# Kernel optimization log

Hardware: AMD Instinct MI355X
Metric: run time of the kernel (lower is better)

The kernel has to match this reference:

```python
import jax, jax.numpy as jnp
import numpy as np

HIDDEN = 2048
HEADS = 16
HEAD_DIM = HIDDEN // HEADS
BLOCK = 64
SEQ = 4096
NUM_BLOCKS = SEQ // BLOCK
N_LOCAL = 3
N_GLOBAL = 1
N_RANDOM = 1
SCALE = 1.0 / np.sqrt(HEAD_DIM)


def _sparse_mask(rand_idx):
    # rand_idx: [num_blocks, n_random] int -- random key-block per query-block row
    i = jnp.arange(NUM_BLOCKS)[:, None]
    j = jnp.arange(NUM_BLOCKS)[None, :]
    half = N_LOCAL // 2
    local = (j >= i - half) & (j <= i + half)
    glob = (j < N_GLOBAL) | (j >= NUM_BLOCKS - N_GLOBAL)
    rand = jnp.any(j[:, :, None] == rand_idx[:, None, :], axis=-1)
    blk = local | glob | rand                      # [nb, nb] bool
    full = jnp.repeat(jnp.repeat(blk, BLOCK, axis=0), BLOCK, axis=1)
    return full[:SEQ, :SEQ]                        # [S, S] bool


def setup_inputs() -> dict:
    key = jax.random.key(0)
    k1, k2, k3, k4, k5, k6 = jax.random.split(key, 6)
    s = 0.02
    return {
        "hidden_states": jax.random.normal(k1, (1, SEQ, HIDDEN), jnp.float32),
        "rand_idx": jax.random.randint(k2, (NUM_BLOCKS, N_RANDOM), 0, NUM_BLOCKS, jnp.int32),
        "Wq": jax.random.normal(k3, (HIDDEN, HIDDEN), jnp.float32) * s,
        "Wk": jax.random.normal(k4, (HIDDEN, HIDDEN), jnp.float32) * s,
        "Wv": jax.random.normal(k5, (HIDDEN, HIDDEN), jnp.float32) * s,
        "Wo": jax.random.normal(k6, (HIDDEN, HIDDEN), jnp.float32) * s,
    }


def reference(hidden_states, rand_idx, Wq, Wk, Wv, Wo):
    B, S, _ = hidden_states.shape
    # torch Linear: y = x @ W.T
    q = (hidden_states @ Wq.T).reshape(B, S, HEADS, HEAD_DIM).transpose(0, 2, 1, 3)
    k = (hidden_states @ Wk.T).reshape(B, S, HEADS, HEAD_DIM).transpose(0, 2, 1, 3)
    v = (hidden_states @ Wv.T).reshape(B, S, HEADS, HEAD_DIM).transpose(0, 2, 1, 3)
    scores = jnp.einsum("bhqd,bhkd->bhqk", q, k) * SCALE
    mask = _sparse_mask(rand_idx)                  # [S, S] bool
    scores = jnp.where(mask[None, None, :, :], scores, -jnp.inf)
    probs = jax.nn.softmax(scores, axis=-1)
    out = jnp.einsum("bhqk,bhkd->bhqd", probs, v)
    out = out.transpose(0, 2, 1, 3).reshape(B, S, HIDDEN)
    return out @ Wo.T
```

## Files before the change

### kernel.cpp

```cpp
#include <hip/hip_runtime.h>

typedef unsigned short u16;
typedef __bf16 bf16x8 __attribute__((ext_vector_type(8)));
typedef float f32x4 __attribute__((ext_vector_type(4)));

#define SEQQ 4096
#define HID 2048
#define HD 128
#define NBLK 64
#define ATT_SCALE 0.08838834764831843f

__device__ __forceinline__ u16 f2bf(float f) {
    unsigned u = __float_as_uint(f);
    u += 0x7fffu + ((u >> 16) & 1u);
    return (u16)(u >> 16);
}

__device__ __forceinline__ void gload_lds16(const void* g, void* l) {
    __builtin_amdgcn_global_load_lds((const __attribute__((address_space(1))) void*)g,
                                     (__attribute__((address_space(3))) void*)l, 16, 0, 0);
}

__global__ __launch_bounds__(256) void cvt_bf16_k(const float* __restrict__ in,
                                                  u16* __restrict__ out, int n4) {
    int i = blockIdx.x * 256 + threadIdx.x;
    if (i < n4) {
        float4 v = ((const float4*)in)[i];
        ushort4 o;
        o.x = f2bf(v.x); o.y = f2bf(v.y); o.z = f2bf(v.z); o.w = f2bf(v.w);
        ((ushort4*)out)[i] = o;
    }
}

__global__ __launch_bounds__(256) void cvt4_k(const float* __restrict__ w0,
                                              const float* __restrict__ w1,
                                              const float* __restrict__ w2,
                                              const float* __restrict__ w3,
                                              u16* __restrict__ qkv,
                                              u16* __restrict__ wo) {
    const int y = blockIdx.y;
    const float* src = (y == 0) ? w0 : (y == 1) ? w1 : (y == 2) ? w2 : w3;
    u16* dst = (y < 3) ? (qkv + (size_t)y * 4194304) : wo;
    int i = blockIdx.x * 256 + threadIdx.x;
    float4 v = ((const float4*)src)[i];
    ushort4 o;
    o.x = f2bf(v.x); o.y = f2bf(v.y); o.z = f2bf(v.z); o.w = f2bf(v.w);
    ((ushort4*)dst)[i] = o;
}

template <int MODE>
__global__ __launch_bounds__(256) void gemm_bt(const u16* __restrict__ A,
                                               const u16* __restrict__ B,
                                               void* __restrict__ C,
                                               int M, int N, int K) {
    __shared__ __align__(16) u16 As[128 * 32];
    __shared__ __align__(16) u16 Bs[128 * 32];
    const int t = threadIdx.x, w = t >> 6, l = t & 63;
    const int lg = l >> 4, ll = l & 15;

    const int gx = gridDim.x, gy = gridDim.y;
    const int nwg = gx * gy;
    int lid = blockIdx.y * gx + blockIdx.x;
    int swz = (lid & 7) * (nwg >> 3) + (lid >> 3);
    const int mb = swz % gy;
    const int nb = swz / gy;

    const int wr = w >> 1, wc = w & 1;

    f32x4 acc[4][4] = {};

    const int sr = l >> 2;
    const int sc = (l & 3) * 8;
    const u16* gA = A + (size_t)(mb * 128 + w * 16 + sr) * K + sc;
    const u16* gB = B + (size_t)(nb * 128 + w * 16 + sr) * K + sc;
    char* lA0 = (char*)As + w * 1024;
    char* lA1 = (char*)As + (w + 4) * 1024;
    char* lB0 = (char*)Bs + w * 1024;
    char* lB1 = (char*)Bs + (w + 4) * 1024;

    for (int kt = 0; kt < K; kt += 32) {
        __syncthreads();
        gload_lds16(gA + kt, lA0);
        gload_lds16(gA + (size_t)64 * K + kt, lA1);
        gload_lds16(gB + kt, lB0);
        gload_lds16(gB + (size_t)64 * K + kt, lB1);
        __syncthreads();

        bf16x8 af[4], bfr[4];
#pragma unroll
        for (int mi = 0; mi < 4; ++mi)
            af[mi] = *(const bf16x8*)&As[(wr * 64 + mi * 16 + ll) * 32 + lg * 8];
#pragma unroll
        for (int ni = 0; ni < 4; ++ni)
            bfr[ni] = *(const bf16x8*)&Bs[(wc * 64 + ni * 16 + ll) * 32 + lg * 8];
#pragma unroll
        for (int mi = 0; mi < 4; ++mi)
#pragma unroll
            for (int ni = 0; ni < 4; ++ni)
                acc[mi][ni] = __builtin_amdgcn_mfma_f32_16x16x32_bf16(af[mi], bfr[ni],
                                                                      acc[mi][ni], 0, 0, 0);
    }

    const int row0 = mb * 128 + wr * 64, col0 = nb * 128 + wc * 64;
#pragma unroll
    for (int mi = 0; mi < 4; ++mi)
#pragma unroll
        for (int ni = 0; ni < 4; ++ni) {
            f32x4 v = acc[mi][ni];
#pragma unroll
            for (int r = 0; r < 4; ++r) {
                int row = row0 + mi * 16 + lg * 4 + r;
                int col = col0 + ni * 16 + ll;
                if (MODE == 0) {
                    ((float*)C)[(size_t)row * N + col] = v[r];
                } else {
                    u16* Cq = (u16*)C;
                    if (col < 2048)
                        Cq[(size_t)row * 2048 + col] = f2bf(v[r]);
                    else if (col < 4096)
                        Cq[8388608 + (size_t)row * 2048 + (col - 2048)] = f2bf(v[r]);
                    else
                        Cq[16777216 + (size_t)(col - 4096) * 4096 + row] = f2bf(v[r]);
                }
            }
        }
}

__global__ __launch_bounds__(256) void sparse_attn(const u16* __restrict__ Q,
                                                   const u16* __restrict__ Kmat,
                                                   const u16* __restrict__ Vt,
                                                   const int* __restrict__ rnd,
                                                   u16* __restrict__ Out) {
    __shared__ __align__(16) u16 Ks[2][8192];
    __shared__ __align__(16) u16 Vs[2][8192];
    __shared__ __align__(16) char Plds[4 * 2048];

    const int qb = blockIdx.x, h = blockIdx.y;
    const int t = threadIdx.x, w = t >> 6, l = t & 63;
    const int lg = l >> 4, ll = l & 15;

    int blist[6];
    int nblk = 0;
    {
        int cands[6];
        cands[0] = qb - 1; cands[1] = qb; cands[2] = qb + 1;
        cands[3] = 0; cands[4] = NBLK - 1; cands[5] = rnd[qb];
        for (int c = 0; c < 6; ++c) {
            int b = cands[c];
            if (b < 0 || b >= NBLK) continue;
            bool dup = false;
            for (int j = 0; j < nblk; ++j) dup = dup || (blist[j] == b);
            if (!dup) blist[nblk++] = b;
        }
    }

    auto stage = [&](int buf, int kb) {
        const u16* kbase = Kmat + (size_t)(kb * 64) * HID + h * HD;
        const u16* vbase = Vt + (size_t)(h * HD) * SEQQ + kb * 64;
#pragma unroll
        for (int j = 0; j < 4; ++j) {
            int d = j * 256 + t;
            int kr = d >> 4, kc_ = (d & 15) ^ (kr & 7);
            gload_lds16(kbase + (size_t)kr * HID + kc_ * 8, &Ks[buf][d * 8]);
            int vr = d >> 3, vc = (d & 7) ^ (vr & 7);
            gload_lds16(vbase + (size_t)vr * SEQQ + vc * 8, &Vs[buf][d * 8]);
        }
    };

    bf16x8 qf[4];
    const int qrow = qb * 64 + w * 16 + ll;
#pragma unroll
    for (int kc = 0; kc < 4; ++kc)
        qf[kc] = *(const bf16x8*)&Q[(size_t)qrow * HID + h * HD + kc * 32 + lg * 8];

    f32x4 o[8];
#pragma unroll
    for (int dt = 0; dt < 8; ++dt) o[dt] = (f32x4){0.f, 0.f, 0.f, 0.f};
    float mrun[4], lrun[4];
#pragma unroll
    for (int r = 0; r < 4; ++r) { mrun[r] = -1e30f; lrun[r] = 0.f; }

    char* Pw = Plds + w * 2048;

    stage(0, blist[0]);
    int cur = 0;

    for (int bi = 0; bi < nblk; ++bi) {
        if (bi + 1 < nblk) {
            stage(cur ^ 1, blist[bi + 1]);
            asm volatile("s_waitcnt vmcnt(8)\n\ts_barrier" ::: "memory");
        } else {
            asm volatile("s_waitcnt vmcnt(0)\n\ts_barrier" ::: "memory");
        }

        f32x4 s[4];
#pragma unroll
        for (int ct = 0; ct < 4; ++ct) s[ct] = (f32x4){0.f, 0.f, 0.f, 0.f};
#pragma unroll
        for (int ct = 0; ct < 4; ++ct) {
            const int krow = ct * 16 + ll;
#pragma unroll
            for (int kc = 0; kc < 4; ++kc) {
                bf16x8 kf = *(const bf16x8*)&Ks[cur][krow * 128 +
                                                    (((kc * 4 + lg) ^ (krow & 7)) << 3)];
                s[ct] = __builtin_amdgcn_mfma_f32_16x16x32_bf16(qf[kc], kf, s[ct], 0, 0, 0);
            }
        }

        float rmax[4];
#pragma unroll
        for (int r = 0; r < 4; ++r) {
            s[0][r] *= ATT_SCALE; s[1][r] *= ATT_SCALE;
            s[2][r] *= ATT_SCALE; s[3][r] *= ATT_SCALE;
            rmax[r] = fmaxf(fmaxf(s[0][r], s[1][r]), fmaxf(s[2][r], s[3][r]));
        }
#pragma unroll
        for (int mk = 1; mk <= 8; mk <<= 1)
#pragma unroll
            for (int r = 0; r < 4; ++r)
                rmax[r] = fmaxf(rmax[r], __shfl_xor(rmax[r], mk));

        float scl[4], psum[4];
#pragma unroll
        for (int r = 0; r < 4; ++r) {
            float mn = fmaxf(mrun[r], rmax[r]);
            scl[r] = __expf(mrun[r] - mn);
            mrun[r] = mn;
            psum[r] = 0.f;
        }

#pragma unroll
        for (int ct = 0; ct < 4; ++ct)
#pragma unroll
            for (int r = 0; r < 4; ++r) {
                float e = __expf(s[ct][r] - mrun[r]);
                psum[r] += e;
                const int q = lg * 4 + r;
                const int kv = ct * 16 + ll;
                *(u16*)(Pw + q * 128 + ((kv * 2) ^ ((q & 7) << 4))) = f2bf(e);
            }
#pragma unroll
        for (int mk = 1; mk <= 8; mk <<= 1)
#pragma unroll
            for (int r = 0; r < 4; ++r)
                psum[r] += __shfl_xor(psum[r], mk);
#pragma unroll
        for (int r = 0; r < 4; ++r)
            lrun[r] = lrun[r] * scl[r] + psum[r];
#pragma unroll
        for (int dt = 0; dt < 8; ++dt)
#pragma unroll
            for (int r = 0; r < 4; ++r)
                o[dt][r] *= scl[r];

#pragma unroll
        for (int kc2 = 0; kc2 < 2; ++kc2) {
            bf16x8 pf = *(const bf16x8*)(Pw + ll * 128 +
                                         ((kc2 * 64 + lg * 16) ^ ((ll & 7) << 4)));
#pragma unroll
            for (int dt = 0; dt < 8; ++dt) {
                const int vrow = dt * 16 + ll;
                bf16x8 vf = *(const bf16x8*)&Vs[cur][vrow * 64 +
                                                     (((kc2 * 4 + lg) ^ (vrow & 7)) << 3)];
                o[dt] = __builtin_amdgcn_mfma_f32_16x16x32_bf16(pf, vf, o[dt], 0, 0, 0);
            }
        }

        asm volatile("s_barrier" ::: "memory");
        cur ^= 1;
    }

    float rl[4];
#pragma unroll
    for (int r = 0; r < 4; ++r) rl[r] = 1.f / lrun[r];
#pragma unroll
    for (int dt = 0; dt < 8; ++dt)
#pragma unroll
        for (int r = 0; r < 4; ++r) {
            int row = qb * 64 + w * 16 + lg * 4 + r;
            int col = h * HD + dt * 16 + ll;
            Out[(size_t)row * HID + col] = f2bf(o[dt][r] * rl[r]);
        }
}

extern "C" void kernel_launch(void* const* d_in, const int* in_sizes, int n_in,
                              void* d_out, int out_size, void* d_ws, size_t ws_size,
                              hipStream_t stream) {
    const float* hs = (const float*)d_in[0];
    const int* rnd = (const int*)d_in[1];
    const float* Wq = (const float*)d_in[2];
    const float* Wk = (const float*)d_in[3];
    const float* Wv = (const float*)d_in[4];
    const float* Wo = (const float*)d_in[5];
    float* out = (float*)d_out;

    char* ws = (char*)d_ws;
    u16* hs_b   = (u16*)(ws);
    u16* Wqkv_b = (u16*)(ws + 16777216);
    u16* Wo_b   = (u16*)(ws + 41943040);
    u16* Qb     = (u16*)(ws + 50331648);
    u16* Kb     = (u16*)(ws + 67108864);
    u16* Vtb    = (u16*)(ws + 83886080);
    u16* Ab     = (u16*)(ws + 100663296);

    cvt_bf16_k<<<dim3(8192), 256, 0, stream>>>(hs, hs_b, 8388608 / 4);
    cvt4_k<<<dim3(4096, 4), 256, 0, stream>>>(Wq, Wk, Wv, Wo, Wqkv_b, Wo_b);

    gemm_bt<3><<<dim3(48, 32), 256, 0, stream>>>(hs_b, Wqkv_b, Qb, 4096, 6144, 2048);

    sparse_attn<<<dim3(64, 16), 256, 0, stream>>>(Qb, Kb, Vtb, rnd, Ab);

    gemm_bt<0><<<dim3(16, 32), 256, 0, stream>>>(Ab, Wo_b, out, 4096, 2048, 2048);
}
```

Baseline: 417.5 us.

## Replace GEMM with 256x256 double-buffered 8-wave kernel and separate V transpose

```diff
diff --git a/kernel.cpp b/kernel.cpp
--- a/kernel.cpp
+++ b/kernel.cpp
@@ -1,6 +1,7 @@
 #include <hip/hip_runtime.h>
 
 typedef unsigned short u16;
+typedef unsigned short u16x8 __attribute__((ext_vector_type(8)));
 typedef __bf16 bf16x8 __attribute__((ext_vector_type(8)));
 typedef float f32x4 __attribute__((ext_vector_type(4)));
 
@@ -48,82 +49,147 @@
     ((ushort4*)dst)[i] = o;
 }
 
+#define QUAD(MH, AF, BF)                                                        \
+    __builtin_amdgcn_s_setprio(1);                                              \
+    _Pragma("unroll") for (int mi = 0; mi < 4; ++mi) {                          \
+        _Pragma("unroll") for (int ni = 0; ni < 4; ++ni)                        \
+            acc[(MH) * 4 + mi][ni] = __builtin_amdgcn_mfma_f32_16x16x32_bf16(   \
+                (AF)[mi], (BF)[ni], acc[(MH) * 4 + mi][ni], 0, 0, 0);           \
+    }                                                                           \
+    __builtin_amdgcn_s_setprio(0);
+
 template <int MODE>
-__global__ __launch_bounds__(256) void gemm_bt(const u16* __restrict__ A,
-                                               const u16* __restrict__ B,
-                                               void* __restrict__ C,
-                                               int M, int N, int K) {
-    __shared__ __align__(16) u16 As[128 * 32];
-    __shared__ __align__(16) u16 Bs[128 * 32];
+__global__ __launch_bounds__(512, 2) void gemm256(const u16* __restrict__ A,
+                                                  const u16* __restrict__ B,
+                                                  void* __restrict__ C0,
+                                                  u16* __restrict__ C1,
+                                                  u16* __restrict__ C2,
+                                                  int M, int N, int K) {
+    __shared__ __align__(16) u16 As[2][2][4][256][8];
+    __shared__ __align__(16) u16 Bs[2][2][4][256][8];
     const int t = threadIdx.x, w = t >> 6, l = t & 63;
-    const int lg = l >> 4, ll = l & 15;
+    const int wm = w >> 2, wn = w & 3, ll = l & 15, lg = l >> 4;
 
     const int gx = gridDim.x, gy = gridDim.y;
     const int nwg = gx * gy;
     int lid = blockIdx.y * gx + blockIdx.x;
     int swz = (lid & 7) * (nwg >> 3) + (lid >> 3);
-    const int mb = swz % gy;
-    const int nb = swz / gy;
-
-    const int wr = w >> 1, wc = w & 1;
-
-    f32x4 acc[4][4] = {};
-
-    const int sr = l >> 2;
-    const int sc = (l & 3) * 8;
-    const u16* gA = A + (size_t)(mb * 128 + w * 16 + sr) * K + sc;
-    const u16* gB = B + (size_t)(nb * 128 + w * 16 + sr) * K + sc;
-    char* lA0 = (char*)As + w * 1024;
-    char* lA1 = (char*)As + (w + 4) * 1024;
-    char* lB0 = (char*)Bs + w * 1024;
-    char* lB1 = (char*)Bs + (w + 4) * 1024;
-
-    for (int kt = 0; kt < K; kt += 32) {
-        __syncthreads();
-        gload_lds16(gA + kt, lA0);
-        gload_lds16(gA + (size_t)64 * K + kt, lA1);
-        gload_lds16(gB + kt, lB0);
-        gload_lds16(gB + (size_t)64 * K + kt, lB1);
-        __syncthreads();
-
-        bf16x8 af[4], bfr[4];
+    const int mb = swz % gy, nb = swz / gy;
+
+    const int c1 = t, c2 = t + 512;
+    const u16* gA1 = A + (size_t)(mb * 256 + (c1 & 255)) * K + (c1 >> 8) * 8;
+    const u16* gA2 = A + (size_t)(mb * 256 + (c2 & 255)) * K + (c2 >> 8) * 8;
+    const u16* gB1 = B + (size_t)(nb * 256 + (c1 & 255)) * K + (c1 >> 8) * 8;
+    const u16* gB2 = B + (size_t)(nb * 256 + (c2 & 255)) * K + (c2 >> 8) * 8;
+
+    f32x4 acc[8][4] = {};
+
+    auto stageA = [&](int buf, int kh, int kt) {
+        gload_lds16(gA1 + kt * 64 + kh * 32, &As[buf][kh][c1 >> 8][c1 & 255][0]);
+        gload_lds16(gA2 + kt * 64 + kh * 32, &As[buf][kh][c2 >> 8][c2 & 255][0]);
+    };
+    auto stageB = [&](int buf, int kh, int kt) {
+        gload_lds16(gB1 + kt * 64 + kh * 32, &Bs[buf][kh][c1 >> 8][c1 & 255][0]);
+        gload_lds16(gB2 + kt * 64 + kh * 32, &Bs[buf][kh][c2 >> 8][c2 & 255][0]);
+    };
+    auto fragsA = [&](int buf, int kh, int mh, bf16x8* af) {
 #pragma unroll
         for (int mi = 0; mi < 4; ++mi)
-            af[mi] = *(const bf16x8*)&As[(wr * 64 + mi * 16 + ll) * 32 + lg * 8];
+            af[mi] = *(const bf16x8*)&As[buf][kh][lg][wm * 128 + mh * 64 + mi * 16 + ll][0];
+    };
+    auto fragsB = [&](int buf, int kh, bf16x8* bf) {
 #pragma unroll
         for (int ni = 0; ni < 4; ++ni)
-            bfr[ni] = *(const bf16x8*)&Bs[(wc * 64 + ni * 16 + ll) * 32 + lg * 8];
-#pragma unroll
-        for (int mi = 0; mi < 4; ++mi)
-#pragma unroll
-            for (int ni = 0; ni < 4; ++ni)
-                acc[mi][ni] = __builtin_amdgcn_mfma_f32_16x16x32_bf16(af[mi], bfr[ni],
-                                                                      acc[mi][ni], 0, 0, 0);
-    }
-
-    const int row0 = mb * 128 + wr * 64, col0 = nb * 128 + wc * 64;
-#pragma unroll
-    for (int mi = 0; mi < 4; ++mi)
+            bf[ni] = *(const bf16x8*)&Bs[buf][kh][lg][wn * 64 + ni * 16 + ll][0];
+    };
+
+    stageA(0, 0, 0); stageB(0, 0, 0); stageA(0, 1, 0); stageB(0, 1, 0);
+    asm volatile("s_waitcnt vmcnt(4)" ::: "memory");
+    asm volatile("s_barrier" ::: "memory");
+
+    const int T = K >> 6;
+    for (int kt = 0; kt < T; ++kt) {
+        const int buf = kt & 1, nbuf = buf ^ 1;
+        const bool last = (kt == T - 1);
+        bf16x8 a0[4], a1[4], b0[4];
+        fragsA(buf, 0, 0, a0); fragsB(buf, 0, b0);
+        if (!last) stageA(nbuf, 0, kt + 1);
+        asm volatile("s_barrier" ::: "memory");
+        QUAD(0, a0, b0)
+        asm volatile("s_barrier" ::: "memory");
+        fragsA(buf, 0, 1, a1);
+        if (!last) {
+            stageB(nbuf, 0, kt + 1);
+            asm volatile("s_waitcnt vmcnt(4)" ::: "memory");
+        } else {
+            asm volatile("s_waitcnt vmcnt(0)" ::: "memory");
+        }
+        asm volatile("s_barrier" ::: "memory");
+        QUAD(1, a1, b0)
+        asm volatile("s_barrier" ::: "memory");
+        fragsA(buf, 1, 0, a0); fragsB(buf, 1, b0);
+        if (!last) stageA(nbuf, 1, kt + 1);
+        asm volatile("s_barrier" ::: "memory");
+        QUAD(0, a0, b0)
+        asm volatile("s_barrier" ::: "memory");
+        fragsA(buf, 1, 1, a1);
+        if (!last) {
+            stageB(nbuf, 1, kt + 1);
+            asm volatile("s_waitcnt vmcnt(4)" ::: "memory");
+        }
+        asm volatile("s_barrier" ::: "memory");
+        QUAD(1, a1, b0)
+        asm volatile("s_barrier" ::: "memory");
+    }
+
+    const int colb = nb * 256;
+    u16* dstq = nullptr;
+    int coff = 0;
+    if (MODE == 1) {
+        if (colb < 2048)      { dstq = (u16*)C0; coff = colb; }
+        else if (colb < 4096) { dstq = C1; coff = colb - 2048; }
+        else                  { dstq = C2; coff = colb - 4096; }
+    }
+#pragma unroll
+    for (int mi = 0; mi < 8; ++mi)
 #pragma unroll
         for (int ni = 0; ni < 4; ++ni) {
             f32x4 v = acc[mi][ni];
 #pragma unroll
             for (int r = 0; r < 4; ++r) {
-                int row = row0 + mi * 16 + lg * 4 + r;
-                int col = col0 + ni * 16 + ll;
-                if (MODE == 0) {
-                    ((float*)C)[(size_t)row * N + col] = v[r];
-                } else {
-                    u16* Cq = (u16*)C;
-                    if (col < 2048)
-                        Cq[(size_t)row * 2048 + col] = f2bf(v[r]);
-                    else if (col < 4096)
-                        Cq[8388608 + (size_t)row * 2048 + (col - 2048)] = f2bf(v[r]);
-                    else
-                        Cq[16777216 + (size_t)(col - 4096) * 4096 + row] = f2bf(v[r]);
-                }
+                int row = mb * 256 + wm * 128 + mi * 16 + lg * 4 + r;
+                int col = wn * 64 + ni * 16 + ll;
+                if (MODE == 0)
+                    ((float*)C0)[(size_t)row * N + colb + col] = v[r];
+                else
+                    dstq[(size_t)row * 2048 + coff + col] = f2bf(v[r]);
             }
         }
+}
+
+__global__ __launch_bounds__(256) void transpose_k(const u16* __restrict__ in,
+                                                   u16* __restrict__ out) {
+    __shared__ __align__(16) u16 tl[64][64];
+    const int s0 = blockIdx.x * 64, d0 = blockIdx.y * 64;
+    const int t = threadIdx.x;
+#pragma unroll
+    for (int j = 0; j < 2; ++j) {
+        int c = j * 256 + t;
+        int sr = c >> 3, c8 = c & 7;
+        u16x8 v = *(const u16x8*)&in[(size_t)(s0 + sr) * 2048 + d0 + c8 * 8];
+        *(u16x8*)&tl[sr][(c8 ^ (sr >> 3)) * 8] = v;
+    }
+    __syncthreads();
+#pragma unroll
+    for (int j = 0; j < 2; ++j) {
+        int c = j * 256 + t;
+        int dr = c >> 3, sg = c & 7;
+        u16x8 v;
+#pragma unroll
+        for (int i = 0; i < 8; ++i)
+            v[i] = tl[sg * 8 + i][(((dr >> 3) ^ sg) * 8) + (dr & 7)];
+        *(u16x8*)&out[(size_t)(d0 + dr) * 4096 + s0 + sg * 8] = v;
+    }
 }
 
 __global__ __launch_bounds__(256) void sparse_attn(const u16* __restrict__ Q,
@@ -306,9 +372,11 @@
     cvt_bf16_k<<<dim3(8192), 256, 0, stream>>>(hs, hs_b, 8388608 / 4);
     cvt4_k<<<dim3(4096, 4), 256, 0, stream>>>(Wq, Wk, Wv, Wo, Wqkv_b, Wo_b);
 
-    gemm_bt<3><<<dim3(48, 32), 256, 0, stream>>>(hs_b, Wqkv_b, Qb, 4096, 6144, 2048);
+    gemm256<1><<<dim3(24, 16), 512, 0, stream>>>(hs_b, Wqkv_b, Qb, Kb, Ab, 4096, 6144, 2048);
+
+    transpose_k<<<dim3(64, 32), 256, 0, stream>>>(Ab, Vtb);
 
     sparse_attn<<<dim3(64, 16), 256, 0, stream>>>(Qb, Kb, Vtb, rnd, Ab);
 
-    gemm_bt<0><<<dim3(16, 32), 256, 0, stream>>>(Ab, Wo_b, out, 4096, 2048, 2048);
-}
+    gemm256<0><<<dim3(8, 16), 512, 0, stream>>>(Ab, Wo_b, out, nullptr, nullptr, 4096, 2048, 2048);
+}
```

After: 477.0 us. 14.2% more time.
